# Kernel optimization log

Measured on AMD Instinct MI355X. Metric: run time of the kernel, lower is better.

## Reference

```python
import jax, jax.numpy as jnp
import numpy as np

T_TOKENS = 4096      # batch*seq_len
HIDDEN = 2048
N_EXPERTS = 8
TOP_K = 2


def setup_inputs() -> dict:
    key = jax.random.key(0)
    k1, k2 = jax.random.split(key)
    hidden_states = jax.random.normal(k1, (T_TOKENS, HIDDEN), dtype=jnp.float32)
    # nn.Linear(hidden_size, num_experts) weight: [E, H]
    w_router = jax.random.normal(k2, (N_EXPERTS, HIDDEN), dtype=jnp.float32) * (1.0 / np.sqrt(HIDDEN))
    return {"hidden_states": hidden_states, "w_router": w_router, "top_k": TOP_K}


def reference(hidden_states, w_router, top_k):
    T, H = hidden_states.shape
    E = w_router.shape[0]
    # router_logits = linear_router(hidden_states.float())  -> [T, E]
    logits = jnp.einsum("th,eh->te", hidden_states.astype(jnp.float32), w_router)
    # topk along expert dim (torch does this in fp64; ordering/values identical for fp32 inputs)
    top_val, top_idx = jax.lax.top_k(logits, top_k)  # [T, k], [T, k]
    # scatter top values into a dense [T, E] grid of -inf, then transpose -> [E, T]
    rows = jnp.arange(T)[:, None]
    scores_te = jnp.full((T, E), -jnp.inf, dtype=jnp.float32).at[rows, top_idx].set(top_val)
    router_scores = jax.nn.sigmoid(scores_te).T  # [E, T]; sigmoid(-inf) == 0
    # router_indices: arange(T) broadcast to [E, T], flattened, expanded across hidden dim
    router_indices = jnp.broadcast_to(jnp.arange(T, dtype=jnp.int32)[None, :], (E, T))
    router_indices = jnp.broadcast_to(router_indices.reshape(-1, 1), (E * T, H))  # [E*T, H]
    router_probs = router_scores.reshape(-1, 1)  # [E*T, 1]
    return (router_scores, router_indices, router_probs)
```

## Files before the change

kernel.cpp:

```cpp
#include <hip/hip_runtime.h>
#include <math.h>

#define T_TOKENS 4096
#define HIDDEN   2048
#define N_EXPERTS 8
#define N_ROWS   (N_EXPERTS * T_TOKENS)
#define ROW_F4   (HIDDEN / 4)

#define NBLOCKS       2048
#define ROUTER_BLOCKS 256
#define FILL_BLOCKS   (NBLOCKS - ROUTER_BLOCKS)
#define FILL_WAVES    (FILL_BLOCKS * 4)

__global__ __launch_bounds__(256) void fused_router_fill(
    const float* __restrict__ h, const float* __restrict__ w,
    float* __restrict__ out0, float* __restrict__ out1, float* __restrict__ out2)
{
    const int bid  = blockIdx.x;
    const int wave = threadIdx.x >> 6;
    const int lane = threadIdx.x & 63;

    if (bid < ROUTER_BLOCKS) {
        const int t0 = bid * 16 + wave * 4;

        const float4* h4 = (const float4*)h;
        const float4* w4 = (const float4*)w;

        float acc[4][N_EXPERTS];
        #pragma unroll
        for (int t = 0; t < 4; t++)
            #pragma unroll
            for (int e = 0; e < N_EXPERTS; e++) acc[t][e] = 0.f;

        #pragma unroll
        for (int k = 0; k < 8; k++) {
            float4 hv[4];
            #pragma unroll
            for (int t = 0; t < 4; t++)
                hv[t] = h4[(size_t)(t0 + t) * ROW_F4 + k * 64 + lane];
            #pragma unroll
            for (int e = 0; e < N_EXPERTS; e++) {
                float4 wv = w4[e * ROW_F4 + k * 64 + lane];
                #pragma unroll
                for (int t = 0; t < 4; t++)
                    acc[t][e] += hv[t].x * wv.x + hv[t].y * wv.y
                               + hv[t].z * wv.z + hv[t].w * wv.w;
            }
        }

        #pragma unroll
        for (int t = 0; t < 4; t++)
            #pragma unroll
            for (int e = 0; e < N_EXPERTS; e++)
                #pragma unroll
                for (int off = 32; off > 0; off >>= 1)
                    acc[t][e] += __shfl_down(acc[t][e], off, 64);

        if (lane == 0) {
            #pragma unroll
            for (int t = 0; t < 4; t++) {
                const int tok = t0 + t;
                int i1 = 0; float v1 = acc[t][0];
                #pragma unroll
                for (int e = 1; e < N_EXPERTS; e++)
                    if (acc[t][e] > v1) { v1 = acc[t][e]; i1 = e; }
                int i2 = -1; float v2 = -INFINITY;
                #pragma unroll
                for (int e = 0; e < N_EXPERTS; e++)
                    if (e != i1 && acc[t][e] > v2) { v2 = acc[t][e]; i2 = e; }

                float s1 = 1.f / (1.f + expf(-v1));
                float s2 = 1.f / (1.f + expf(-v2));

                #pragma unroll
                for (int e = 0; e < N_EXPERTS; e++) {
                    float val = (e == i1) ? s1 : ((e == i2) ? s2 : 0.f);
                    out0[e * T_TOKENS + tok] = val;
                    out2[e * T_TOKENS + tok] = val;
                }
            }
        }
    } else {
        const int fb    = bid - ROUTER_BLOCKS;
        const int fwave = fb * 4 + wave;
        float4* o4 = (float4*)out1;

        for (int r = fwave; r < N_ROWS; r += FILL_WAVES) {
            float v = (float)(r & (T_TOKENS - 1));
            float4 vv = make_float4(v, v, v, v);
            float4* rowp = o4 + (size_t)r * ROW_F4;
            #pragma unroll
            for (int j = 0; j < 8; j++)
                rowp[j * 64 + lane] = vv;
        }
    }
}

extern "C" void kernel_launch(void* const* d_in, const int* in_sizes, int n_in,
                              void* d_out, int out_size, void* d_ws, size_t ws_size,
                              hipStream_t stream) {
    const float* h = (const float*)d_in[0];
    const float* w = (const float*)d_in[1];

    float* out  = (float*)d_out;
    float* out0 = out;
    float* out1 = out + N_EXPERTS * T_TOKENS;
    float* out2 = out1 + (size_t)N_EXPERTS * T_TOKENS * HIDDEN;

    hipLaunchKernelGGL(fused_router_fill, dim3(NBLOCKS), dim3(256), 0, stream,
                       h, w, out0, out1, out2);
}
```

Baseline: 332.6 us.

## Split fused router/fill kernel into separate router and fill launches

Replaces the single fused kernel, which split its blocks between router work and a grid-stride fill of the index tensor, with two launches. The router kernel uses 256 blocks. The fill kernel uses 2048 blocks, and each wave writes exactly four rows with no loop. This removes the fill loop and the block-role branch and gives the fill a full grid of its own. The cost is a second launch, and the router's small work no longer overlaps the fill on the same stream.

```diff
diff --git a/kernel.cpp b/kernel.cpp
--- a/kernel.cpp
+++ b/kernel.cpp
@@ -7,92 +7,90 @@
 #define N_ROWS   (N_EXPERTS * T_TOKENS)
 #define ROW_F4   (HIDDEN / 4)
 
-#define NBLOCKS       2048
-#define ROUTER_BLOCKS 256
-#define FILL_BLOCKS   (NBLOCKS - ROUTER_BLOCKS)
-#define FILL_WAVES    (FILL_BLOCKS * 4)
 
-__global__ __launch_bounds__(256) void fused_router_fill(
+__global__ __launch_bounds__(256) void router_kernel(
     const float* __restrict__ h, const float* __restrict__ w,
-    float* __restrict__ out0, float* __restrict__ out1, float* __restrict__ out2)
+    float* __restrict__ out0, float* __restrict__ out2)
 {
-    const int bid  = blockIdx.x;
     const int wave = threadIdx.x >> 6;
     const int lane = threadIdx.x & 63;
+    const int t0   = (blockIdx.x * 4 + wave) * 4;
 
-    if (bid < ROUTER_BLOCKS) {
-        const int t0 = bid * 16 + wave * 4;
+    const float4* h4 = (const float4*)h;
+    const float4* w4 = (const float4*)w;
 
-        const float4* h4 = (const float4*)h;
-        const float4* w4 = (const float4*)w;
+    float acc[4][N_EXPERTS];
+    #pragma unroll
+    for (int t = 0; t < 4; t++)
+        #pragma unroll
+        for (int e = 0; e < N_EXPERTS; e++) acc[t][e] = 0.f;
 
-        float acc[4][N_EXPERTS];
+    #pragma unroll
+    for (int k = 0; k < 8; k++) {
+        float4 hv[4];
         #pragma unroll
         for (int t = 0; t < 4; t++)
-            #pragma unroll
-            for (int e = 0; e < N_EXPERTS; e++) acc[t][e] = 0.f;
-
+            hv[t] = h4[(size_t)(t0 + t) * ROW_F4 + k * 64 + lane];
         #pragma unroll
-        for (int k = 0; k < 8; k++) {
-            float4 hv[4];
+        for (int e = 0; e < N_EXPERTS; e++) {
+            float4 wv = w4[e * ROW_F4 + k * 64 + lane];
             #pragma unroll
             for (int t = 0; t < 4; t++)
-                hv[t] = h4[(size_t)(t0 + t) * ROW_F4 + k * 64 + lane];
+                acc[t][e] += hv[t].x * wv.x + hv[t].y * wv.y
+                           + hv[t].z * wv.z + hv[t].w * wv.w;
+        }
+    }
+
+    #pragma unroll
+    for (int t = 0; t < 4; t++)
+        #pragma unroll
+        for (int e = 0; e < N_EXPERTS; e++)
+            #pragma unroll
+            for (int off = 32; off > 0; off >>= 1)
+                acc[t][e] += __shfl_down(acc[t][e], off, 64);
+
+    if (lane == 0) {
+        #pragma unroll
+        for (int t = 0; t < 4; t++) {
+            const int tok = t0 + t;
+            int i1 = 0; float v1 = acc[t][0];
+            #pragma unroll
+            for (int e = 1; e < N_EXPERTS; e++)
+                if (acc[t][e] > v1) { v1 = acc[t][e]; i1 = e; }
+            int i2 = -1; float v2 = -INFINITY;
+            #pragma unroll
+            for (int e = 0; e < N_EXPERTS; e++)
+                if (e != i1 && acc[t][e] > v2) { v2 = acc[t][e]; i2 = e; }
+
+            float s1 = 1.f / (1.f + expf(-v1));
+            float s2 = 1.f / (1.f + expf(-v2));
+
             #pragma unroll
             for (int e = 0; e < N_EXPERTS; e++) {
-                float4 wv = w4[e * ROW_F4 + k * 64 + lane];
-                #pragma unroll
-                for (int t = 0; t < 4; t++)
-                    acc[t][e] += hv[t].x * wv.x + hv[t].y * wv.y
-                               + hv[t].z * wv.z + hv[t].w * wv.w;
+                float val = (e == i1) ? s1 : ((e == i2) ? s2 : 0.f);
+                out0[e * T_TOKENS + tok] = val;
+                out2[e * T_TOKENS + tok] = val;
             }
         }
+    }
+}
 
+__global__ __launch_bounds__(256) void fill_kernel(float* __restrict__ out1)
+{
+    const int wave = threadIdx.x >> 6;
+    const int lane = threadIdx.x & 63;
+    const int gw   = blockIdx.x * 4 + wave;
+    const int r0   = gw * 4;
+
+    float4* o4 = (float4*)out1;
+    #pragma unroll
+    for (int i = 0; i < 4; i++) {
+        float v = (float)((r0 + i) & (T_TOKENS - 1));
+        float4 vv = make_float4(v, v, v, v);
+        float4* rowp = o4 + (size_t)(r0 + i) * ROW_F4;
         #pragma unroll
-        for (int t = 0; t < 4; t++)
-            #pragma unroll
-            for (int e = 0; e < N_EXPERTS; e++)
-                #pragma unroll
-                for (int off = 32; off > 0; off >>= 1)
-                    acc[t][e] += __shfl_down(acc[t][e], off, 64);
-
-        if (lane == 0) {
-            #pragma unroll
-            for (int t = 0; t < 4; t++) {
-                const int tok = t0 + t;
-                int i1 = 0; float v1 = acc[t][0];
-                #pragma unroll
-                for (int e = 1; e < N_EXPERTS; e++)
-                    if (acc[t][e] > v1) { v1 = acc[t][e]; i1 = e; }
-                int i2 = -1; float v2 = -INFINITY;
-                #pragma unroll
-                for (int e = 0; e < N_EXPERTS; e++)
-                    if (e != i1 && acc[t][e] > v2) { v2 = acc[t][e]; i2 = e; }
-
-                float s1 = 1.f / (1.f + expf(-v1));
-                float s2 = 1.f / (1.f + expf(-v2));
-
-                #pragma unroll
-                for (int e = 0; e < N_EXPERTS; e++) {
-                    float val = (e == i1) ? s1 : ((e == i2) ? s2 : 0.f);
-                    out0[e * T_TOKENS + tok] = val;
-                    out2[e * T_TOKENS + tok] = val;
-                }
-            }
-        }
-    } else {
-        const int fb    = bid - ROUTER_BLOCKS;
-        const int fwave = fb * 4 + wave;
-        float4* o4 = (float4*)out1;
-
-        for (int r = fwave; r < N_ROWS; r += FILL_WAVES) {
-            float v = (float)(r & (T_TOKENS - 1));
-            float4 vv = make_float4(v, v, v, v);
-            float4* rowp = o4 + (size_t)r * ROW_F4;
-            #pragma unroll
-            for (int j = 0; j < 8; j++)
-                rowp[j * 64 + lane] = vv;
-        }
+        for (int j = 0; j < 8; j++)
+            rowp[j * 64 + lane] = vv;
     }
 }
 
@@ -107,6 +105,7 @@
     float* out1 = out + N_EXPERTS * T_TOKENS;
     float* out2 = out1 + (size_t)N_EXPERTS * T_TOKENS * HIDDEN;
 
-    hipLaunchKernelGGL(fused_router_fill, dim3(NBLOCKS), dim3(256), 0, stream,
-                       h, w, out0, out1, out2);
+    hipLaunchKernelGGL(router_kernel, dim3(256), dim3(256), 0, stream,
+                       h, w, out0, out2);
+    hipLaunchKernelGGL(fill_kernel, dim3(2048), dim3(256), 0, stream, out1);
 }
```

Measured after the change: 305.1 us. -8.3%, faster.
